# Kernel tuning notes

Hardware: AMD Instinct MI355X
Metric: run time of the kernel (lower is better)

## Reference

```python
import jax, jax.numpy as jnp
import numpy as np

N_NODES = 100000
N_EDGES = 1600000
IN_CH = 1024
FEAT_CH = 128
OUT_CH = 3


def setup_inputs() -> dict:
    key = jax.random.key(0)
    ks = jax.random.split(key, 9)
    features = jax.random.normal(ks[0], (N_NODES, IN_CH), dtype=jnp.float32)
    edges = jax.random.randint(ks[1], (2, N_EDGES), 0, N_NODES, dtype=jnp.int64)
    edges2 = jax.random.randint(ks[2], (2, N_EDGES), 0, N_NODES, dtype=jnp.int64)
    edge_features = jax.random.normal(ks[3], (N_EDGES, 1), dtype=jnp.float32)
    additional_feature = jax.random.normal(ks[4], (N_NODES, 20), dtype=jnp.float32)
    # GCNConv linear weights (glorot-ish scale) and biases
    W1 = jax.random.normal(ks[5], (IN_CH, FEAT_CH), dtype=jnp.float32) * (1.0 / np.sqrt(IN_CH))
    b1 = jnp.zeros((FEAT_CH,), dtype=jnp.float32)
    W2 = jax.random.normal(ks[6], (FEAT_CH, OUT_CH), dtype=jnp.float32) * (1.0 / np.sqrt(FEAT_CH))
    b2 = jnp.zeros((OUT_CH,), dtype=jnp.float32)
    return {"features": features, "edges": edges, "edges2": edges2,
            "edge_features": edge_features, "additional_feature": additional_feature,
            "W1": W1, "b1": b1, "W2": W2, "b2": b2}


def gcn_conv(x, edge_index, W, b, num_nodes):
    """PyG GCNConv: x' = D^{-1/2}(A+I)D^{-1/2} x W + b (self-loops added)."""
    x = x @ W  # project first (cheaper feature dim for aggregation)
    loop = jnp.arange(num_nodes, dtype=edge_index.dtype)
    src = jnp.concatenate([edge_index[0], loop])
    dst = jnp.concatenate([edge_index[1], loop])
    deg = jax.ops.segment_sum(jnp.ones_like(dst, dtype=x.dtype), dst,
                              num_segments=num_nodes)  # >=1 due to self-loops
    dinv = jax.lax.rsqrt(deg)
    norm = dinv[src] * dinv[dst]  # [E+N]
    out = jax.ops.segment_sum(x[src] * norm[:, None], dst, num_segments=num_nodes)
    return out + b


def reference(features, edges, edges2, edge_features, additional_feature, W1, b1, W2, b2):
    # use_additional_channels=False -> features unchanged; edge_features forced to None
    n = features.shape[0]
    x = gcn_conv(features, edges2, W1, b1, n)
    x = jax.nn.relu(x)
    # dropout inactive in eval mode
    return gcn_conv(x, edges2, W2, b2, n)
```

## Files before the change

### kernel.cpp

```cpp
#include <hip/hip_runtime.h>
#include <hip/hip_bf16.h>

typedef __attribute__((ext_vector_type(8))) _Float16 half8;
typedef __attribute__((ext_vector_type(4))) _Float16 half4;
typedef __attribute__((ext_vector_type(4))) float f32x4;

#define N_NODES 100000
#define N_EDGES 1600000
#define IN_CH 1024
#define FEAT 128
#define CAP 64
#define NDIG 196
#define CAPC 10240
#define NTILES ((N_NODES + 127) / 128)

__device__ __forceinline__ int swz(int row, int colbyte) {
    return row * 128 + (colbyte ^ ((row & 7) << 4));
}

__global__ void k_prep(const float* __restrict__ W1, _Float16* __restrict__ W1t,
                       int* __restrict__ cursorC, int* __restrict__ done) {
    int idx = blockIdx.x * 256 + threadIdx.x;
    if (idx < IN_CH * FEAT) {
        int col = idx & (FEAT - 1), k = idx >> 7;
        W1t[(size_t)col * IN_CH + k] = (_Float16)W1[idx];
    }
    if (idx < NDIG) cursorC[idx] = idx * CAPC;
    if (idx == 0) *done = 0;
}

__global__ __launch_bounds__(256, 2) void k_build_gemm(
    const float* __restrict__ A, const _Float16* __restrict__ Bt,
    const int4* __restrict__ src4, const int4* __restrict__ dst4,
    int* __restrict__ cursorC, uint2* __restrict__ recs,
    int* __restrict__ csr, int* __restrict__ cnt, float* __restrict__ dinvarr,
    int* __restrict__ done, _Float16* __restrict__ H, int M, int e4)
{
    __shared__ union {
        struct { _Float16 As[2][128 * 64]; _Float16 Bsw[2][128 * 64]; } g;
        struct { int hist[NDIG], segoff[NDIG], lcur[NDIG]; } bin;
        int cl[512];
    } sm;
    const int t = threadIdx.x;

    if (blockIdx.x < NDIG) {
        const int b = blockIdx.x;
        if (t < NDIG) sm.bin.hist[t] = 0;
        __syncthreads();
        const int base4 = b * 2048;
        int4 sv[8], dv[8];
#pragma unroll
        for (int j = 0; j < 8; ++j) {
            int idx = base4 + j * 256 + t;
            if (idx < e4) { sv[j] = src4[idx]; dv[j] = dst4[idx]; }
            else { sv[j] = (int4){-1,-1,-1,-1}; dv[j] = (int4){-1,-1,-1,-1}; }
        }
#pragma unroll
        for (int j = 0; j < 8; ++j) {
            int dd[4] = {dv[j].x, dv[j].y, dv[j].z, dv[j].w};
            int ss[4] = {sv[j].x, sv[j].y, sv[j].z, sv[j].w};
#pragma unroll
            for (int c = 0; c < 4; ++c)
                if ((unsigned)dd[c] < N_NODES && (unsigned)ss[c] < N_NODES)
                    atomicAdd(&sm.bin.hist[dd[c] >> 9], 1);
        }
        __syncthreads();
        if (t < NDIG) {
            sm.bin.segoff[t] = atomicAdd(&cursorC[t], sm.bin.hist[t]);
            sm.bin.lcur[t] = 0;
        }
        __syncthreads();
#pragma unroll
        for (int j = 0; j < 8; ++j) {
            int dd[4] = {dv[j].x, dv[j].y, dv[j].z, dv[j].w};
            int ss[4] = {sv[j].x, sv[j].y, sv[j].z, sv[j].w};
#pragma unroll
            for (int c = 0; c < 4; ++c) {
                if ((unsigned)dd[c] < N_NODES && (unsigned)ss[c] < N_NODES) {
                    int dg = dd[c] >> 9;
                    int r = atomicAdd(&sm.bin.lcur[dg], 1);
                    int pos = sm.bin.segoff[dg] + r;
                    if (pos < (dg + 1) * CAPC)
                        recs[pos] = (uint2){(unsigned)ss[c], (unsigned)dd[c]};
                }
            }
        }
        __syncthreads();
        if (t == 0) {
            __threadfence();
            __hip_atomic_fetch_add(done, 1, __ATOMIC_RELEASE, __HIP_MEMORY_SCOPE_AGENT);
            while (__hip_atomic_load(done, __ATOMIC_ACQUIRE, __HIP_MEMORY_SCOPE_AGENT) < NDIG)
                __builtin_amdgcn_s_sleep(8);
        }
        __syncthreads();
        const int d = blockIdx.x;
        for (int j = t; j < 512; j += 256) sm.cl[j] = 0;
        __syncthreads();
        const int base = d * CAPC;
        int n = cursorC[d] - base;
        if (n > CAPC) n = CAPC;
        for (int k = t; k < n; k += 256) {
            uint2 r = recs[base + k];
            int local = (int)r.y & 511;
            int slot = atomicAdd(&sm.cl[local], 1);
            if (slot < CAP) csr[((int)r.y << 6) + slot] = (int)r.x;
        }
        __syncthreads();
        const int node0 = d << 9;
        for (int j = t; j < 512; j += 256) {
            int node = node0 + j;
            if (node < N_NODES) {
                int c = sm.cl[j] < CAP ? sm.cl[j] : CAP;
                cnt[node] = c;
                dinvarr[node] = rsqrtf((float)(c + 1));
            }
        }
        return;
    }

    const int wid = t >> 6, lane = t & 63;
    const int brow0 = (blockIdx.x - NDIG) * 128;

    f32x4 acc[2][8];
#pragma unroll
    for (int m = 0; m < 2; ++m)
#pragma unroll
        for (int nn = 0; nn < 8; ++nn) acc[m][nn] = (f32x4){0.f, 0.f, 0.f, 0.f};

    const int sarow = t >> 4;
    const int sacolB = (t & 15) * 8;
    const float* paBase[8];
#pragma unroll
    for (int i = 0; i < 8; ++i) {
        int grow = brow0 + i * 16 + sarow;
        if (grow >= M) grow = M - 1;
        paBase[i] = A + (size_t)grow * IN_CH + (t & 15) * 4;
    }
    const int bcol = t >> 1;
    const int bhalf = (t & 1) * 64;
    const _Float16* pb = Bt + (size_t)bcol * IN_CH + (t & 1) * 32;

    float4 areg[8];
    half8 bst[4];

#define LOAD_AB(kt)                                                             \
    {                                                                           \
        _Pragma("unroll") for (int i = 0; i < 8; ++i)                           \
            areg[i] = *(const float4*)(paBase[i] + (kt) * 64);                  \
        const half8* s_ = (const half8*)(pb + (kt) * 64);                       \
        _Pragma("unroll") for (int j = 0; j < 4; ++j) bst[j] = s_[j];           \
    }
#define CVT_WRITE(buf)                                                          \
    {                                                                           \
        _Pragma("unroll") for (int i = 0; i < 8; ++i) {                         \
            half4 h;                                                            \
            h[0] = (_Float16)areg[i].x; h[1] = (_Float16)areg[i].y;             \
            h[2] = (_Float16)areg[i].z; h[3] = (_Float16)areg[i].w;             \
            *(half4*)((char*)sm.g.As[buf] + swz(i * 16 + sarow, sacolB)) = h;   \
        }                                                                       \
        _Pragma("unroll") for (int j = 0; j < 4; ++j)                           \
            *(half8*)((char*)sm.g.Bsw[buf] + swz(bcol, bhalf + j * 16)) = bst[j]; \
    }
#define MFMA_STEP(cur)                                                          \
    {                                                                           \
        _Pragma("unroll") for (int kk = 0; kk < 2; ++kk) {                      \
            const int cb = kk * 64 + (lane >> 4) * 16;                          \
            half8 a0 = *(const half8*)((char*)sm.g.As[cur] + swz(wid * 32 + (lane & 15), cb)); \
            half8 a1 = *(const half8*)((char*)sm.g.As[cur] + swz(wid * 32 + 16 + (lane & 15), cb)); \
            _Pragma("unroll") for (int nn = 0; nn < 8; ++nn) {                  \
                half8 bb = *(const half8*)((char*)sm.g.Bsw[cur] + swz(nn * 16 + (lane & 15), cb)); \
                acc[0][nn] = __builtin_amdgcn_mfma_f32_16x16x32_f16(a0, bb, acc[0][nn], 0, 0, 0); \
                acc[1][nn] = __builtin_amdgcn_mfma_f32_16x16x32_f16(a1, bb, acc[1][nn], 0, 0, 0); \
            }                                                                   \
        }                                                                       \
    }

    LOAD_AB(0);
    CVT_WRITE(0);
    __syncthreads();

#pragma unroll 1
    for (int kt = 0; kt < 16; ++kt) {
        const int cur = kt & 1;
        if (kt + 1 < 16) LOAD_AB(kt + 1);
        MFMA_STEP(cur);
        if (kt + 1 < 16) {
            CVT_WRITE(cur ^ 1);
            __syncthreads();
        }
    }
#undef LOAD_AB
#undef CVT_WRITE
#undef MFMA_STEP

    int colb = lane & 15, rgrp = (lane >> 4) * 4;
#pragma unroll
    for (int m = 0; m < 2; ++m) {
#pragma unroll
        for (int r = 0; r < 4; ++r) {
            int grow = brow0 + wid * 32 + m * 16 + rgrp + r;
            if (grow < M) {
                _Float16* hp = H + (size_t)grow * FEAT + colb;
#pragma unroll
                for (int nn = 0; nn < 8; ++nn) hp[nn * 16] = (_Float16)acc[m][nn][r];
            }
        }
    }
}

__global__ __launch_bounds__(256) void k_agg1(const _Float16* __restrict__ H,
                                              const int* __restrict__ csr,
                                              const int* __restrict__ cnt,
                                              const float* __restrict__ dinvarr,
                                              const float* __restrict__ b1,
                                              const float* __restrict__ W2,
                                              float* __restrict__ Y, int n) {
    int wid = threadIdx.x >> 6, lane = threadIdx.x & 63;
    int i = blockIdx.x * 4 + wid;
    if (i >= n) return;
    const int g = lane >> 4, u = lane & 15;
    int m = cnt[i];
    float di = dinvarr[i];

    int sl; float dl;
    if (lane < m) { sl = csr[(i << 6) + lane]; dl = dinvarr[sl]; }
    else          { sl = i;                    dl = (lane == m) ? di : 0.f; }
    int mm = (m < 63 ? m : 63) + 1;

    float ax[8];
#pragma unroll
    for (int j = 0; j < 8; ++j) ax[j] = 0.f;

    for (int e = 0; e < mm; e += 16) {
        int idx0 = e + g, idx1 = e + 4 + g, idx2 = e + 8 + g, idx3 = e + 12 + g;
        bool v0 = idx0 < mm, v1 = idx1 < mm, v2 = idx2 < mm, v3 = idx3 < mm;
        int c0i = v0 ? idx0 : 0, c1i = v1 ? idx1 : 0;
        int c2i = v2 ? idx2 : 0, c3i = v3 ? idx3 : 0;
        int s0 = __shfl(sl, c0i); float w0 = __shfl(dl, c0i);
        int s1 = __shfl(sl, c1i); float w1 = __shfl(dl, c1i);
        int s2 = __shfl(sl, c2i); float w2 = __shfl(dl, c2i);
        int s3 = __shfl(sl, c3i); float w3 = __shfl(dl, c3i);
        if (!v0) { s0 = i; w0 = 0.f; }
        if (!v1) { s1 = i; w1 = 0.f; }
        if (!v2) { s2 = i; w2 = 0.f; }
        if (!v3) { s3 = i; w3 = 0.f; }
        half8 h0 = *(const half8*)(H + ((size_t)s0 << 7) + u * 8);
        half8 h1 = *(const half8*)(H + ((size_t)s1 << 7) + u * 8);
        half8 h2 = *(const half8*)(H + ((size_t)s2 << 7) + u * 8);
        half8 h3 = *(const half8*)(H + ((size_t)s3 << 7) + u * 8);
#pragma unroll
        for (int j = 0; j < 8; ++j)
            ax[j] += w0 * (float)h0[j] + w1 * (float)h1[j]
                   + w2 * (float)h2[j] + w3 * (float)h3[j];
    }

#pragma unroll
    for (int j = 0; j < 8; ++j) {
        ax[j] += __shfl_xor(ax[j], 16);
        ax[j] += __shfl_xor(ax[j], 32);
    }

    int c0 = u * 8;
    float y0 = 0.f, y1 = 0.f, y2 = 0.f;
#pragma unroll
    for (int j = 0; j < 8; ++j) {
        float x = di * ax[j] + b1[c0 + j];
        x = x > 0.f ? x : 0.f;
        y0 += x * W2[(c0 + j) * 3 + 0];
        y1 += x * W2[(c0 + j) * 3 + 1];
        y2 += x * W2[(c0 + j) * 3 + 2];
    }
#pragma unroll
    for (int d = 1; d < 16; d <<= 1) {
        y0 += __shfl_xor(y0, d);
        y1 += __shfl_xor(y1, d);
        y2 += __shfl_xor(y2, d);
    }
    if (lane == 0) {
        float* yp = Y + (size_t)i * 4;
        yp[0] = di * y0; yp[1] = di * y1; yp[2] = di * y2;
    }
}

__global__ void k_agg2(const float* __restrict__ Y, const int* __restrict__ csr,
                       const int* __restrict__ cnt, const float* __restrict__ dinvarr,
                       const float* __restrict__ b2, float* __restrict__ out, int n) {
    int i = blockIdx.x * 256 + threadIdx.x;
    if (i >= n) return;
    int m = cnt[i];
    float di = dinvarr[i];
    int base = i << 6;
    const float4* Y4 = (const float4*)Y;
    float4 self = Y4[i];
    float a0 = self.x, a1 = self.y, a2 = self.z;
    int e = 0;
    for (; e + 3 < m; e += 4) {
        int s0 = csr[base + e],     s1 = csr[base + e + 1];
        int s2 = csr[base + e + 2], s3 = csr[base + e + 3];
        float4 v0 = Y4[s0], v1 = Y4[s1], v2 = Y4[s2], v3 = Y4[s3];
        a0 += (v0.x + v1.x) + (v2.x + v3.x);
        a1 += (v0.y + v1.y) + (v2.y + v3.y);
        a2 += (v0.z + v1.z) + (v2.z + v3.z);
    }
    for (; e < m; ++e) {
        float4 v0 = Y4[csr[base + e]];
        a0 += v0.x; a1 += v0.y; a2 += v0.z;
    }
    out[(size_t)i * 3 + 0] = di * a0 + b2[0];
    out[(size_t)i * 3 + 1] = di * a1 + b2[1];
    out[(size_t)i * 3 + 2] = di * a2 + b2[2];
}

extern "C" void kernel_launch(void* const* d_in, const int* in_sizes, int n_in,
                              void* d_out, int out_size, void* d_ws, size_t ws_size,
                              hipStream_t stream) {
    const float* features = (const float*)d_in[0];
    const int* edges2 = (const int*)d_in[2];
    const float* W1 = (const float*)d_in[5];
    const float* b1 = (const float*)d_in[6];
    const float* W2 = (const float*)d_in[7];
    const float* b2 = (const float*)d_in[8];
    float* out = (float*)d_out;

    const int N = N_NODES, E = N_EDGES;
    const int4* src4 = (const int4*)edges2;
    const int4* dst4 = (const int4*)(edges2 + E);
    int e4 = E / 4;

    char* p = (char*)d_ws;
    auto carve = [&](size_t bytes) { char* q = p; p += (bytes + 255) & ~(size_t)255; return q; };
    int* cnt       = (int*)carve(4 * (size_t)N);
    float* dinvarr = (float*)carve(4 * (size_t)N);
    int* cursorC   = (int*)carve(4 * NDIG);
    int* done      = (int*)carve(4);
    uint2* recs    = (uint2*)carve(8 * (size_t)NDIG * CAPC);
    int* csr       = (int*)carve(4 * (size_t)N * CAP);
    _Float16* W1t  = (_Float16*)carve(2 * (size_t)IN_CH * FEAT);
    _Float16* H    = (_Float16*)carve(2 * (size_t)N * FEAT);
    float* Y       = (float*)carve(16 * (size_t)N);

    k_prep<<<dim3(512), dim3(256), 0, stream>>>(W1, W1t, cursorC, done);
    k_build_gemm<<<dim3(NDIG + NTILES), dim3(256), 0, stream>>>(
        features, W1t, src4, dst4, cursorC, recs, csr, cnt, dinvarr, done, H, N, e4);
    k_agg1<<<dim3((N + 3) / 4), dim3(256), 0, stream>>>(H, csr, cnt, dinvarr, b1, W2, Y, N);
    k_agg2<<<dim3((N + 255) / 256), dim3(256), 0, stream>>>(Y, csr, cnt, dinvarr, b2, out, N);
}
```

Baseline: 252.6 us.

## Restructure GEMM into 32-row blocks with full-K LDS A tile and fragment-packed B

The GEMM part of the build kernel changes from 128x128 tiles with a double-buffered K loop to 32-row blocks. Each block stages the whole 32x1024 A slab into LDS as fp16 once, then runs the MFMA loop over all of K. W1 is now pre-packed into MFMA fragment order, so B fragments are read directly from global memory (L2-resident) with no LDS staging and no per-step barriers. This brings more blocks and fewer syncs, but B is re-read from L2 by every block and each wave keeps fewer accumulators, so arithmetic intensity per block drops.

```diff
diff --git a/kernel.cpp b/kernel.cpp
--- a/kernel.cpp
+++ b/kernel.cpp
@@ -12,32 +12,36 @@
 #define CAP 64
 #define NDIG 196
 #define CAPC 10240
-#define NTILES ((N_NODES + 127) / 128)
-
-__device__ __forceinline__ int swz(int row, int colbyte) {
-    return row * 128 + (colbyte ^ ((row & 7) << 4));
-}
-
-__global__ void k_prep(const float* __restrict__ W1, _Float16* __restrict__ W1t,
+#define MROWS 32
+#define NGB (N_NODES / MROWS)
+
+__device__ __forceinline__ int swzA(int row, int kbyte) {
+    return row * 2048 + (kbyte ^ ((row & 7) << 4) ^ (((kbyte >> 8) & 7) << 4));
+}
+
+__global__ void k_prep(const float* __restrict__ W1, _Float16* __restrict__ Bf,
                        int* __restrict__ cursorC, int* __restrict__ done) {
     int idx = blockIdx.x * 256 + threadIdx.x;
     if (idx < IN_CH * FEAT) {
         int col = idx & (FEAT - 1), k = idx >> 7;
-        W1t[(size_t)col * IN_CH + k] = (_Float16)W1[idx];
+        int ct = col >> 4, ks = k >> 5;
+        int lane = ((k >> 3) & 3) * 16 + (col & 15);
+        int e = k & 7;
+        Bf[(((ct * 32 + ks) * 64 + lane) << 3) + e] = (_Float16)W1[idx];
     }
     if (idx < NDIG) cursorC[idx] = idx * CAPC;
     if (idx == 0) *done = 0;
 }
 
 __global__ __launch_bounds__(256, 2) void k_build_gemm(
-    const float* __restrict__ A, const _Float16* __restrict__ Bt,
+    const float* __restrict__ A, const _Float16* __restrict__ Bf,
     const int4* __restrict__ src4, const int4* __restrict__ dst4,
     int* __restrict__ cursorC, uint2* __restrict__ recs,
     int* __restrict__ csr, int* __restrict__ cnt, float* __restrict__ dinvarr,
     int* __restrict__ done, _Float16* __restrict__ H, int M, int e4)
 {
     __shared__ union {
-        struct { _Float16 As[2][128 * 64]; _Float16 Bsw[2][128 * 64]; } g;
+        _Float16 As[MROWS * IN_CH];
         struct { int hist[NDIG], segoff[NDIG], lcur[NDIG]; } bin;
         int cl[512];
     } sm;
@@ -118,91 +122,65 @@
         return;
     }
 
+    const int gb = blockIdx.x - NDIG;
+    const int brow0 = gb * MROWS;
     const int wid = t >> 6, lane = t & 63;
-    const int brow0 = (blockIdx.x - NDIG) * 128;
-
-    f32x4 acc[2][8];
-#pragma unroll
-    for (int m = 0; m < 2; ++m)
-#pragma unroll
-        for (int nn = 0; nn < 8; ++nn) acc[m][nn] = (f32x4){0.f, 0.f, 0.f, 0.f};
-
-    const int sarow = t >> 4;
-    const int sacolB = (t & 15) * 8;
-    const float* paBase[8];
-#pragma unroll
-    for (int i = 0; i < 8; ++i) {
-        int grow = brow0 + i * 16 + sarow;
-        if (grow >= M) grow = M - 1;
-        paBase[i] = A + (size_t)grow * IN_CH + (t & 15) * 4;
-    }
-    const int bcol = t >> 1;
-    const int bhalf = (t & 1) * 64;
-    const _Float16* pb = Bt + (size_t)bcol * IN_CH + (t & 1) * 32;
-
-    float4 areg[8];
-    half8 bst[4];
-
-#define LOAD_AB(kt)                                                             \
-    {                                                                           \
-        _Pragma("unroll") for (int i = 0; i < 8; ++i)                           \
-            areg[i] = *(const float4*)(paBase[i] + (kt) * 64);                  \
-        const half8* s_ = (const half8*)(pb + (kt) * 64);                       \
-        _Pragma("unroll") for (int j = 0; j < 4; ++j) bst[j] = s_[j];           \
-    }
-#define CVT_WRITE(buf)                                                          \
-    {                                                                           \
-        _Pragma("unroll") for (int i = 0; i < 8; ++i) {                         \
-            half4 h;                                                            \
-            h[0] = (_Float16)areg[i].x; h[1] = (_Float16)areg[i].y;             \
-            h[2] = (_Float16)areg[i].z; h[3] = (_Float16)areg[i].w;             \
-            *(half4*)((char*)sm.g.As[buf] + swz(i * 16 + sarow, sacolB)) = h;   \
-        }                                                                       \
-        _Pragma("unroll") for (int j = 0; j < 4; ++j)                           \
-            *(half8*)((char*)sm.g.Bsw[buf] + swz(bcol, bhalf + j * 16)) = bst[j]; \
-    }
-#define MFMA_STEP(cur)                                                          \
-    {                                                                           \
-        _Pragma("unroll") for (int kk = 0; kk < 2; ++kk) {                      \
-            const int cb = kk * 64 + (lane >> 4) * 16;                          \
-            half8 a0 = *(const half8*)((char*)sm.g.As[cur] + swz(wid * 32 + (lane & 15), cb)); \
-            half8 a1 = *(const half8*)((char*)sm.g.As[cur] + swz(wid * 32 + 16 + (lane & 15), cb)); \
-            _Pragma("unroll") for (int nn = 0; nn < 8; ++nn) {                  \
-                half8 bb = *(const half8*)((char*)sm.g.Bsw[cur] + swz(nn * 16 + (lane & 15), cb)); \
-                acc[0][nn] = __builtin_amdgcn_mfma_f32_16x16x32_f16(a0, bb, acc[0][nn], 0, 0, 0); \
-                acc[1][nn] = __builtin_amdgcn_mfma_f32_16x16x32_f16(a1, bb, acc[1][nn], 0, 0, 0); \
-            }                                                                   \
-        }                                                                       \
-    }
-
-    LOAD_AB(0);
-    CVT_WRITE(0);
+
+    {
+        const int row = t >> 3;
+        const int c0 = (t & 7) * 128;
+        int grow = brow0 + row; if (grow >= M) grow = M - 1;
+        const float* pa = A + (size_t)grow * IN_CH + c0;
+#pragma unroll
+        for (int ch = 0; ch < 4; ++ch) {
+            float4 v[8];
+#pragma unroll
+            for (int j = 0; j < 8; ++j) v[j] = *(const float4*)(pa + ch * 32 + j * 4);
+#pragma unroll
+            for (int j = 0; j < 8; ++j) {
+                half4 h;
+                h[0] = (_Float16)v[j].x; h[1] = (_Float16)v[j].y;
+                h[2] = (_Float16)v[j].z; h[3] = (_Float16)v[j].w;
+                int kbyte = (c0 + ch * 32 + j * 4) * 2;
+                *(half4*)((char*)sm.As + swzA(row, kbyte)) = h;
+            }
+        }
+    }
     __syncthreads();
 
-#pragma unroll 1
-    for (int kt = 0; kt < 16; ++kt) {
-        const int cur = kt & 1;
-        if (kt + 1 < 16) LOAD_AB(kt + 1);
-        MFMA_STEP(cur);
-        if (kt + 1 < 16) {
-            CVT_WRITE(cur ^ 1);
-            __syncthreads();
-        }
-    }
-#undef LOAD_AB
-#undef CVT_WRITE
-#undef MFMA_STEP
-
-    int colb = lane & 15, rgrp = (lane >> 4) * 4;
-#pragma unroll
-    for (int m = 0; m < 2; ++m) {
-#pragma unroll
-        for (int r = 0; r < 4; ++r) {
-            int grow = brow0 + wid * 32 + m * 16 + rgrp + r;
-            if (grow < M) {
-                _Float16* hp = H + (size_t)grow * FEAT + colb;
-#pragma unroll
-                for (int nn = 0; nn < 8; ++nn) hp[nn * 16] = (_Float16)acc[m][nn][r];
+    const int rt = wid >> 1;
+    const int ctb = (wid & 1) * 4;
+    const int arow = rt * 16 + (lane & 15);
+    const int asub = (lane >> 4) * 16;
+
+    f32x4 acc[4];
+#pragma unroll
+    for (int c = 0; c < 4; ++c) acc[c] = (f32x4){0.f, 0.f, 0.f, 0.f};
+
+    const _Float16* bfl = Bf + lane * 8;
+
+#pragma unroll 4
+    for (int ks = 0; ks < 32; ++ks) {
+        half8 a = *(const half8*)((char*)sm.As + swzA(arow, ks * 64 + asub));
+        half8 b0 = *(const half8*)(bfl + (((ctb + 0) * 32 + ks) << 9));
+        half8 b1 = *(const half8*)(bfl + (((ctb + 1) * 32 + ks) << 9));
+        half8 b2 = *(const half8*)(bfl + (((ctb + 2) * 32 + ks) << 9));
+        half8 b3 = *(const half8*)(bfl + (((ctb + 3) * 32 + ks) << 9));
+        acc[0] = __builtin_amdgcn_mfma_f32_16x16x32_f16(a, b0, acc[0], 0, 0, 0);
+        acc[1] = __builtin_amdgcn_mfma_f32_16x16x32_f16(a, b1, acc[1], 0, 0, 0);
+        acc[2] = __builtin_amdgcn_mfma_f32_16x16x32_f16(a, b2, acc[2], 0, 0, 0);
+        acc[3] = __builtin_amdgcn_mfma_f32_16x16x32_f16(a, b3, acc[3], 0, 0, 0);
+    }
+
+    {
+        int colb = lane & 15, rgrp = (lane >> 4) * 4;
+#pragma unroll
+        for (int c = 0; c < 4; ++c) {
+            int gcol = (ctb + c) * 16 + colb;
+#pragma unroll
+            for (int r = 0; r < 4; ++r) {
+                int grow = brow0 + rt * 16 + rgrp + r;
+                if (grow < M) H[(size_t)grow * FEAT + gcol] = (_Float16)acc[c][r];
             }
         }
     }
@@ -335,13 +313,13 @@
     int* done      = (int*)carve(4);
     uint2* recs    = (uint2*)carve(8 * (size_t)NDIG * CAPC);
     int* csr       = (int*)carve(4 * (size_t)N * CAP);
-    _Float16* W1t  = (_Float16*)carve(2 * (size_t)IN_CH * FEAT);
+    _Float16* Bf   = (_Float16*)carve(2 * (size_t)IN_CH * FEAT);
     _Float16* H    = (_Float16*)carve(2 * (size_t)N * FEAT);
     float* Y       = (float*)carve(16 * (size_t)N);
 
-    k_prep<<<dim3(512), dim3(256), 0, stream>>>(W1, W1t, cursorC, done);
-    k_build_gemm<<<dim3(NDIG + NTILES), dim3(256), 0, stream>>>(
-        features, W1t, src4, dst4, cursorC, recs, csr, cnt, dinvarr, done, H, N, e4);
+    k_prep<<<dim3(512), dim3(256), 0, stream>>>(W1, Bf, cursorC, done);
+    k_build_gemm<<<dim3(NDIG + NGB), dim3(256), 0, stream>>>(
+        features, Bf, src4, dst4, cursorC, recs, csr, cnt, dinvarr, done, H, N, e4);
     k_agg1<<<dim3((N + 3) / 4), dim3(256), 0, stream>>>(H, csr, cnt, dinvarr, b1, W2, Y, N);
     k_agg2<<<dim3((N + 255) / 256), dim3(256), 0, stream>>>(Y, csr, cnt, dinvarr, b2, out, N);
 }
```

New measurement: 302.6 us. 1.2x slower.
